# Optimization experiments

Measured on AMD Instinct MI355X. Metric: run time of the kernel, lower is better.

Reference implementation:

```python
import jax, jax.numpy as jnp
import numpy as np

B, L, D = 8, 2048, 1024
PAD = 512  # trailing padded positions (zeros) to exercise the two padding masks


def setup_inputs() -> dict:
    key = jax.random.key(0)
    ks = jax.random.split(key, 11)
    q = jax.random.normal(ks[0], (B, L, D), dtype=jnp.float32)
    k = jax.random.normal(ks[1], (B, L, D), dtype=jnp.float32)
    v = jax.random.normal(ks[2], (B, L, D), dtype=jnp.float32)
    # zero-pad trailing positions (module infers masks from zero rows)
    q = q.at[:, L - PAD:, :].set(0.0)
    k = k.at[:, L - PAD:, :].set(0.0)
    v = v.at[:, L - PAD:, :].set(0.0)
    s = 1.0 / np.sqrt(D)
    Wq = jax.random.normal(ks[3], (D, D), dtype=jnp.float32) * s
    bq = jax.random.normal(ks[4], (D,), dtype=jnp.float32) * 0.01
    Wk = jax.random.normal(ks[5], (D, D), dtype=jnp.float32) * s
    bk = jax.random.normal(ks[6], (D,), dtype=jnp.float32) * 0.01
    Wv = jax.random.normal(ks[7], (D, D), dtype=jnp.float32) * s
    bv = jax.random.normal(ks[8], (D,), dtype=jnp.float32) * 0.01
    Wo = jax.random.normal(ks[9], (D, D), dtype=jnp.float32) * s
    bo = jax.random.normal(ks[10], (D,), dtype=jnp.float32) * 0.01
    return {"q": q, "k": k, "v": v, "Wq": Wq, "bq": bq, "Wk": Wk, "bk": bk,
            "Wv": Wv, "bv": bv, "Wo": Wo, "bo": bo}


def reference(q, k, v, Wq, bq, Wk, bk, Wv, bv, Wo, bo):
    # masks computed from raw (pre-projection) q, k, exactly like padding_mask_k/_q
    # bmm(ones_like(q), k^T)[b,i,j] == sum_d k[b,j,d]  -> mask where k row sums to 0
    attn_mask = (jnp.sum(k, axis=-1) == 0.0)[:, None, :]      # [B,1,Lk] -> broadcast [B,Lq,Lk]
    softmax_mask = (jnp.sum(q, axis=-1) == 0.0)[:, :, None]    # [B,Lq,1]

    qp = q @ Wq.T + bq  # torch Linear: x W^T + b
    kp = k @ Wk.T + bk
    vp = v @ Wv.T + bv

    scale = vp.shape[-1] ** -0.5  # original overwrites passed `scale`
    att = jnp.einsum('bqd,bkd->bqk', qp, kp) * scale           # [B,Lq,Lk]
    att = jnp.where(attn_mask, -jnp.inf, att)
    att = jax.nn.softmax(att, axis=-1)
    att = jnp.where(softmax_mask, 0.0, att)

    out = jnp.einsum('bqk,bkd->bqd', att, vp)                  # [B,Lq,D]
    out = out @ Wo.T + bo
    x = out + qp  # residual uses the PROJECTED q
    # LayerNorm, elementwise_affine=False, eps=1e-5
    mu = jnp.mean(x, axis=-1, keepdims=True)
    var = jnp.mean(jnp.square(x - mu), axis=-1, keepdims=True)
    return (x - mu) / jnp.sqrt(var + 1e-5)
```

## Files before the change

### kernel.cpp

```cpp
#include <hip/hip_runtime.h>
#include <stdint.h>

typedef unsigned short u16;
typedef __attribute__((ext_vector_type(8))) short short8;
typedef __attribute__((ext_vector_type(4))) float f32x4;

#define B_ 8
#define L_ 2048
#define D_ 1024

__device__ __forceinline__ u16 f2bf(float f) {
    unsigned int u = __float_as_uint(f);
    u = u + 0x7FFFu + ((u >> 16) & 1u);
    return (u16)(u >> 16);
}
__device__ __forceinline__ float bf2f(u16 h) {
    return __uint_as_float(((unsigned int)h) << 16);
}

struct CM3 {
    const float* s[3];
    u16* d[3];
    int* m[3];
};
__global__ __launch_bounds__(256) void convmask3_kernel(CM3 c) {
    int sel = blockIdx.y;
    const float* x = c.s[sel];
    u16* xb = c.d[sel];
    int* mask = c.m[sel];
    long row = blockIdx.x;
    int t = threadIdx.x;
    float4 v = ((const float4*)(x + row * D_))[t];
    ushort4 o;
    o.x = f2bf(v.x); o.y = f2bf(v.y); o.z = f2bf(v.z); o.w = f2bf(v.w);
    ((ushort4*)(xb + row * D_))[t] = o;
    float s = v.x + v.y + v.z + v.w;
    #pragma unroll
    for (int off = 32; off; off >>= 1) s += __shfl_down(s, off);
    __shared__ float sh[4];
    if ((t & 63) == 0) sh[t >> 6] = s;
    __syncthreads();
    if (t == 0) {
        float tot = sh[0] + sh[1] + sh[2] + sh[3];
        mask[row] = (tot == 0.0f) ? 1 : 0;
    }
}

struct Ptr4 { const float* s0; const float* s1; const float* s2; const float* s3; };
__global__ __launch_bounds__(256) void convert4_kernel(Ptr4 p, u16* __restrict__ dst) {
    const float* srcs[4] = {p.s0, p.s1, p.s2, p.s3};
    const float* src = srcs[blockIdx.y];
    u16* d = dst + (size_t)blockIdx.y * D_ * D_;
    int i = blockIdx.x * 256 + threadIdx.x;
    float4 v = ((const float4*)src)[i];
    ushort4 o;
    o.x = f2bf(v.x); o.y = f2bf(v.y); o.z = f2bf(v.z); o.w = f2bf(v.w);
    ((ushort4*)d)[i] = o;
}

__global__ __launch_bounds__(256) void flags_kernel(const int* __restrict__ mq,
                                                    const int* __restrict__ mk,
                                                    const int* __restrict__ mv,
                                                    int* __restrict__ q256,
                                                    int* __restrict__ k256,
                                                    int* __restrict__ v256,
                                                    int* __restrict__ k128,
                                                    int* __restrict__ k32) {
    int b = blockIdx.x, t = threadIdx.x;
    const int* src; int* dst; int g; int n;
    if (b < 64)       { src = mq; dst = q256; g = b;       n = 256; }
    else if (b < 128) { src = mk; dst = k256; g = b - 64;  n = 256; }
    else if (b < 192) { src = mv; dst = v256; g = b - 128; n = 256; }
    else if (b < 320) { src = mk; dst = k128; g = b - 192; n = 128; }
    else              { src = mk; dst = k32;  g = b - 320; n = 32;  }
    int val = (t < n) ? src[(long)g * n + t] : 1;
    __shared__ int sh;
    if (t == 0) sh = 1;
    __syncthreads();
    if (!val) sh = 0;
    __syncthreads();
    if (t == 0) dst[g] = sh;
}

__global__ __launch_bounds__(512) void packbits_kernel(const int* __restrict__ k32,
                                                       unsigned long long* __restrict__ kb) {
    int t = threadIdx.x;
    int b = t >> 6;
    int bit = t & 63;
    unsigned long long m = __ballot(k32[b * 64 + bit] == 0);
    if (bit == 0) kb[b] = m;
}

__device__ __forceinline__ void async_cp16(const void* g, void* l) {
    __builtin_amdgcn_global_load_lds((const __attribute__((address_space(1))) unsigned int*)g,
                                     (__attribute__((address_space(3))) unsigned int*)l,
                                     16, 0, 0);
}

struct P3 {
    const u16* A[3];
    u16* C[3];
    const float* bias[3];
    const int* rs[3];
};

#define GBM 256
#define GBN 256
#define GBK 32

#define STAGE(step, slot)                                                   \
    do {                                                                    \
        const u16* pa_ = gA + (long)(step) * GBK;                           \
        const u16* pb_ = gB + (long)(step) * GBK;                           \
        u16* la_ = &LDS[(slot)][0] + t * 8;                                 \
        async_cp16(pa_, la_);                                               \
        async_cp16(pa_ + 128 * (long)K, la_ + 4096);                        \
        async_cp16(pb_, la_ + 8192);                                        \
        async_cp16(pb_ + 128 * (long)K, la_ + 12288);                       \
    } while (0)

template <int MODE>
__global__ __launch_bounds__(512, 2) void gemm_nt(const u16* __restrict__ A,
                                                  const u16* __restrict__ Bm,
                                                  void* __restrict__ C,
                                                  const float* __restrict__ bias,
                                                  const u16* __restrict__ resid,
                                                  const int* __restrict__ maskk,
                                                  int N, int K,
                                                  long strideA, long strideB, long strideC,
                                                  float scale,
                                                  const int* __restrict__ rowskip,
                                                  const int* __restrict__ colskip,
                                                  const unsigned long long* __restrict__ kbits,
                                                  int mblocks, int nblocks,
                                                  P3 p3) {
    __shared__ __align__(16) u16 LDS[4][16384];

    int t = threadIdx.x;
    int lane = t & 63;
    int wave = t >> 6;
    int wr = wave >> 2;
    int wc = wave & 3;
    long m0 = (long)blockIdx.x * GBM;
    long n0 = (long)blockIdx.y * GBN;

    const u16* Ab;
    const u16* Bb;
    char* Cb;
    const float* biasp = bias;
    const int* rs;
    int rsidx;
    if (MODE == 0) {
        int z = blockIdx.z;
        Ab = p3.A[z];
        Bb = Bm + (long)z * D_ * D_;
        Cb = (char*)p3.C[z];
        biasp = p3.bias[z];
        rs = p3.rs[z];
        rsidx = blockIdx.x;
    } else {
        Ab = A + (long)blockIdx.z * strideA;
        Bb = Bm + (long)blockIdx.z * strideB;
        Cb = (char*)C + (long)blockIdx.z * strideC;
        rs = rowskip;
        rsidx = blockIdx.z * mblocks + blockIdx.x;
    }
    const int* mk = (MODE == 1) ? (maskk + (long)blockIdx.z * N) : nullptr;

    bool skipK = false;
    if (rs && rs[rsidx]) skipK = true;
    if (MODE == 1 && colskip && colskip[blockIdx.z * nblocks + blockIdx.y]) skipK = true;

    f32x4 acc[8][4] = {};

    int srow = t >> 2;
    int kc = ((t & 3) ^ ((t >> 3) & 3)) * 8;
    const u16* gA = Ab + (m0 + srow) * (long)K + kc;
    const u16* gB = Bb + (n0 + srow) * (long)K + kc;

    int sw = ((lane >> 4) ^ ((lane >> 1) & 3)) * 8;
    int arow0 = wr * 128 + (lane & 15);
    int brow0 = wc * 64 + (lane & 15);

    if (!skipK) {
        unsigned long long bs = 0;
        int NT;
        if (MODE == 2) {
            bs = kbits[blockIdx.z];
            NT = __popcll(bs);
        } else {
            NT = K / GBK;
        }

        int npro = NT < 3 ? NT : 3;
        for (int i = 0; i < npro; i++) {
            int st = i;
            if (MODE == 2) { st = __builtin_ctzll(bs); bs &= bs - 1; }
            STAGE(st, i);
        }
        int nstaged = npro;

        for (int tt = 0; tt < NT; tt++) {
            int rem = NT - 1 - tt;
            if (rem > 1)      asm volatile("s_waitcnt vmcnt(8)" ::: "memory");
            else if (rem == 1) asm volatile("s_waitcnt vmcnt(4)" ::: "memory");
            else               asm volatile("s_waitcnt vmcnt(0)" ::: "memory");
            __builtin_amdgcn_s_barrier();
            asm volatile("" ::: "memory");

            if (nstaged < NT) {
                int st = nstaged;
                if (MODE == 2) { st = __builtin_ctzll(bs); bs &= bs - 1; }
                STAGE(st, nstaged & 3);
                nstaged++;
            }

            const u16* As_ = &LDS[tt & 3][0];
            const u16* Bs_ = As_ + 8192;
            short8 bfr[4], af[4];
            #pragma unroll
            for (int j = 0; j < 4; j++)
                bfr[j] = *(const short8*)&Bs_[(brow0 + j * 16) * GBK + sw];
            #pragma unroll
            for (int i = 0; i < 4; i++)
                af[i] = *(const short8*)&As_[(arow0 + i * 16) * GBK + sw];
            __builtin_amdgcn_s_setprio(1);
            #pragma unroll
            for (int i = 0; i < 4; i++)
                #pragma unroll
                for (int j = 0; j < 4; j++)
                    acc[i][j] = __builtin_amdgcn_mfma_f32_16x16x32_bf16(af[i], bfr[j],
                                                                        acc[i][j], 0, 0, 0);
            __builtin_amdgcn_s_setprio(0);
            #pragma unroll
            for (int i = 0; i < 4; i++)
                af[i] = *(const short8*)&As_[(arow0 + 64 + i * 16) * GBK + sw];
            __builtin_amdgcn_s_setprio(1);
            #pragma unroll
            for (int i = 0; i < 4; i++)
                #pragma unroll
                for (int j = 0; j < 4; j++)
                    acc[4 + i][j] = __builtin_amdgcn_mfma_f32_16x16x32_bf16(af[i], bfr[j],
                                                                            acc[4 + i][j], 0, 0, 0);
            __builtin_amdgcn_s_setprio(0);
        }
    }

    long crow0 = m0 + wr * 128;
    long ccol0 = n0 + wc * 64;
    #pragma unroll
    for (int i = 0; i < 8; i++) {
        #pragma unroll
        for (int j = 0; j < 4; j++) {
            long row = crow0 + i * 16 + (lane >> 4) * 4;
            long col = ccol0 + j * 16 + (lane & 15);
            #pragma unroll
            for (int r = 0; r < 4; r++) {
                float vv = acc[i][j][r];
                long rr = row + r;
                if (MODE == 0) {
                    ((u16*)Cb)[rr * N + col] = f2bf(vv + biasp[col]);
                } else if (MODE == 1) {
                    float s = mk[col] ? -1e30f : vv * scale;
                    ((u16*)Cb)[rr * N + col] = f2bf(s);
                } else if (MODE == 2) {
                    ((u16*)Cb)[rr * N + col] = f2bf(vv);
                } else {
                    float x = vv + biasp[col] + bf2f(resid[rr * (long)N + col]);
                    ((u16*)Cb)[rr * N + col] = f2bf(x);
                }
            }
        }
    }
}

__global__ __launch_bounds__(256) void softmax_kernel(const u16* __restrict__ S,
                                                      u16* __restrict__ P,
                                                      const int* __restrict__ maskq) {
    long row = blockIdx.x;
    int t = threadIdx.x;
    const u16* Sr = S + row * L_;
    u16* Pr = P + row * L_;

    if (maskq[row]) {
        short8 z = {};
        *(short8*)&Pr[t * 8] = z;
        return;
    }

    short8 raw = *(const short8*)&Sr[t * 8];
    float s[8];
    #pragma unroll
    for (int e = 0; e < 8; e++) s[e] = bf2f((u16)raw[e]);

    float mx = s[0];
    #pragma unroll
    for (int e = 1; e < 8; e++) mx = fmaxf(mx, s[e]);
    #pragma unroll
    for (int off = 32; off; off >>= 1) mx = fmaxf(mx, __shfl_down(mx, off));
    __shared__ float sh[4];
    if ((t & 63) == 0) sh[t >> 6] = mx;
    __syncthreads();
    mx = fmaxf(fmaxf(sh[0], sh[1]), fmaxf(sh[2], sh[3]));
    __syncthreads();

    float e8[8], sum = 0.f;
    #pragma unroll
    for (int e = 0; e < 8; e++) { e8[e] = __expf(s[e] - mx); sum += e8[e]; }
    #pragma unroll
    for (int off = 32; off; off >>= 1) sum += __shfl_down(sum, off);
    if ((t & 63) == 0) sh[t >> 6] = sum;
    __syncthreads();
    sum = sh[0] + sh[1] + sh[2] + sh[3];
    float inv = 1.0f / sum;

    short8 o;
    #pragma unroll
    for (int e = 0; e < 8; e++) o[e] = (short)f2bf(e8[e] * inv);
    *(short8*)&Pr[t * 8] = o;
}

__global__ __launch_bounds__(256) void transpose_k(const u16* __restrict__ src,
                                                   u16* __restrict__ dst) {
    __shared__ u16 tile[32][34];
    long b = blockIdx.z;
    const u16* s = src + b * (long)L_ * D_;
    u16* d = dst + b * (long)L_ * D_;
    int gx = blockIdx.x * 32;
    int gy = blockIdx.y * 32;
    int tx = threadIdx.x, ty = threadIdx.y;
    #pragma unroll
    for (int r = 0; r < 32; r += 8)
        tile[ty + r][tx] = s[(long)(gy + ty + r) * D_ + gx + tx];
    __syncthreads();
    #pragma unroll
    for (int r = 0; r < 32; r += 8)
        d[(long)(gx + ty + r) * L_ + gy + tx] = tile[tx][ty + r];
}

__global__ __launch_bounds__(256) void layernorm_kernel(const u16* __restrict__ X,
                                                        float* __restrict__ O) {
    long row = blockIdx.x;
    int t = threadIdx.x;
    ushort4 u = ((const ushort4*)(X + row * D_))[t];
    float x0 = bf2f(u.x), x1 = bf2f(u.y), x2 = bf2f(u.z), x3 = bf2f(u.w);
    float s = x0 + x1 + x2 + x3;
    #pragma unroll
    for (int off = 32; off; off >>= 1) s += __shfl_down(s, off);
    __shared__ float sh[4];
    if ((t & 63) == 0) sh[t >> 6] = s;
    __syncthreads();
    float mu = (sh[0] + sh[1] + sh[2] + sh[3]) * (1.0f / D_);
    __syncthreads();

    float d0 = x0 - mu, d1 = x1 - mu, d2 = x2 - mu, d3 = x3 - mu;
    float ss = d0 * d0 + d1 * d1 + d2 * d2 + d3 * d3;
    #pragma unroll
    for (int off = 32; off; off >>= 1) ss += __shfl_down(ss, off);
    if ((t & 63) == 0) sh[t >> 6] = ss;
    __syncthreads();
    float var = (sh[0] + sh[1] + sh[2] + sh[3]) * (1.0f / D_);
    float rs = rsqrtf(var + 1e-5f);

    float4 o;
    o.x = d0 * rs; o.y = d1 * rs; o.z = d2 * rs; o.w = d3 * rs;
    ((float4*)(O + row * D_))[t] = o;
}

extern "C" void kernel_launch(void* const* d_in, const int* in_sizes, int n_in,
                              void* d_out, int out_size, void* d_ws, size_t ws_size,
                              hipStream_t stream) {
    const float* q  = (const float*)d_in[0];
    const float* k  = (const float*)d_in[1];
    const float* v  = (const float*)d_in[2];
    const float* Wq = (const float*)d_in[3];
    const float* bq = (const float*)d_in[4];
    const float* Wk = (const float*)d_in[5];
    const float* bk = (const float*)d_in[6];
    const float* Wv = (const float*)d_in[7];
    const float* bv = (const float*)d_in[8];
    const float* Wo = (const float*)d_in[9];
    const float* bo = (const float*)d_in[10];
    float* out = (float*)d_out;

    char* ws = (char*)d_ws;
    const size_t SZ = (size_t)B_ * L_ * D_ * 2;

    u16* qb   = (u16*)(ws + 0 * SZ);
    u16* kb   = (u16*)(ws + 1 * SZ);
    u16* vb   = (u16*)(ws + 2 * SZ);
    u16* vpb  = (u16*)(ws + 3 * SZ);
    u16* Sbuf = (u16*)(ws + 0 * SZ);
    u16* Pbuf = (u16*)(ws + 2 * SZ);
    u16* Obuf = (u16*)(ws + 0 * SZ);
    u16* Xbuf = (u16*)(ws + 2 * SZ);
    char* p = ws + 4 * SZ;
    u16* qpb = (u16*)p; p += SZ;
    u16* kpb = (u16*)p; p += SZ;
    u16* vpT = (u16*)p; p += SZ;
    u16* Wqb = (u16*)p; p += (size_t)D_ * D_ * 2;
    u16* Wkb = (u16*)p; p += (size_t)D_ * D_ * 2;
    u16* Wvb = (u16*)p; p += (size_t)D_ * D_ * 2;
    u16* Wob = (u16*)p; p += (size_t)D_ * D_ * 2;
    int* maskq = (int*)p; p += (size_t)B_ * L_ * 4;
    int* maskk = (int*)p; p += (size_t)B_ * L_ * 4;
    int* maskv = (int*)p; p += (size_t)B_ * L_ * 4;
    int* q256 = (int*)p; p += 64 * 4;
    int* k256 = (int*)p; p += 64 * 4;
    int* v256 = (int*)p; p += 64 * 4;
    int* kmask128 = (int*)p; p += 128 * 4;
    int* kmask32  = (int*)p; p += 512 * 4;
    unsigned long long* kbits = (unsigned long long*)p; p += 8 * 8;

    P3 noP3 = {};

    CM3 cm;
    cm.s[0] = q;  cm.s[1] = k;  cm.s[2] = v;
    cm.d[0] = qb; cm.d[1] = kb; cm.d[2] = vb;
    cm.m[0] = maskq; cm.m[1] = maskk; cm.m[2] = maskv;
    convmask3_kernel<<<dim3(B_ * L_, 3), 256, 0, stream>>>(cm);
    Ptr4 wp{Wq, Wk, Wv, Wo};
    convert4_kernel<<<dim3(D_ * D_ / 4 / 256, 4), 256, 0, stream>>>(wp, Wqb);
    flags_kernel<<<832, 256, 0, stream>>>(maskq, maskk, maskv, q256, k256, v256, kmask128, kmask32);
    packbits_kernel<<<1, 512, 0, stream>>>(kmask32, kbits);

    P3 pj;
    pj.A[0] = qb;  pj.A[1] = kb;  pj.A[2] = vb;
    pj.C[0] = qpb; pj.C[1] = kpb; pj.C[2] = vpb;
    pj.bias[0] = bq; pj.bias[1] = bk; pj.bias[2] = bv;
    pj.rs[0] = q256; pj.rs[1] = k256; pj.rs[2] = v256;
    gemm_nt<0><<<dim3(B_ * L_ / GBM, D_ / GBN, 3), 512, 0, stream>>>(
        nullptr, Wqb, nullptr, nullptr, nullptr, nullptr, D_, D_, 0, 0, 0, 0.f,
        nullptr, nullptr, nullptr, 0, 4, pj);

    transpose_k<<<dim3(D_ / 32, L_ / 32, B_), dim3(32, 8), 0, stream>>>(vpb, vpT);

    gemm_nt<1><<<dim3(L_ / GBM, L_ / GBN, B_), 512, 0, stream>>>(
        qpb, kpb, Sbuf, nullptr, nullptr, maskk, L_, D_,
        (long)L_ * D_, (long)L_ * D_, (long)L_ * L_ * 2, 0.03125f,
        q256, k256, nullptr, L_ / GBM, L_ / GBN, noP3);

    softmax_kernel<<<B_ * L_, 256, 0, stream>>>(Sbuf, Pbuf, maskq);

    gemm_nt<2><<<dim3(L_ / GBM, D_ / GBN, B_), 512, 0, stream>>>(
        Pbuf, vpT, Obuf, nullptr, nullptr, nullptr, D_, L_,
        (long)L_ * L_, (long)D_ * L_, (long)L_ * D_ * 2, 0.f,
        q256, nullptr, kbits, L_ / GBM, D_ / GBN, noP3);

    gemm_nt<3><<<dim3(B_ * L_ / GBM, D_ / GBN, 1), 512, 0, stream>>>(
        Obuf, Wob, Xbuf, bo, qpb, nullptr, D_, D_, 0, 0, 0, 0.f,
        q256, nullptr, nullptr, B_ * L_ / GBM, D_ / GBN, noP3);

    layernorm_kernel<<<B_ * L_, 256, 0, stream>>>(Xbuf, out);
}
```

Before: 550.7 us.

## Restructure GEMM to BK=64 double-buffered quadrant pipeline with interleaved loads

The GEMM main loop changes from a 4-slot BK=32 ring to a 2-buffer BK=64 scheme. Each wave now computes four 64x32 quadrants, with LDS reads, async global-to-LDS copies and MFMA phases interleaved between barriers, and a new 8-way XOR swizzle. In step with the larger K tile, the skip bitmask is repacked to 32 bits per batch, each bit covering two 32-wide chunks. The aim is more overlap of memory traffic with MFMA work and fewer loop iterations. The cost is more barriers per iteration and fragile waitcnt accounting.

```diff
diff --git a/kernel.cpp b/kernel.cpp
--- a/kernel.cpp
+++ b/kernel.cpp
@@ -82,13 +82,14 @@
     if (t == 0) dst[g] = sh;
 }
 
-__global__ __launch_bounds__(512) void packbits_kernel(const int* __restrict__ k32,
+__global__ __launch_bounds__(256) void packbits_kernel(const int* __restrict__ k32,
                                                        unsigned long long* __restrict__ kb) {
     int t = threadIdx.x;
-    int b = t >> 6;
-    int bit = t & 63;
-    unsigned long long m = __ballot(k32[b * 64 + bit] == 0);
-    if (bit == 0) kb[b] = m;
+    int b = t >> 5;
+    int i = t & 31;
+    bool act = (k32[b * 64 + 2 * i] == 0) || (k32[b * 64 + 2 * i + 1] == 0);
+    unsigned long long m = __ballot(act);
+    if (i == 0) kb[b] = (b & 1) ? (m >> 32) : (m & 0xffffffffULL);
 }
 
 __device__ __forceinline__ void async_cp16(const void* g, void* l) {
@@ -106,17 +107,54 @@
 
 #define GBM 256
 #define GBN 256
-#define GBK 32
-
-#define STAGE(step, slot)                                                   \
-    do {                                                                    \
-        const u16* pa_ = gA + (long)(step) * GBK;                           \
-        const u16* pb_ = gB + (long)(step) * GBK;                           \
-        u16* la_ = &LDS[(slot)][0] + t * 8;                                 \
-        async_cp16(pa_, la_);                                               \
-        async_cp16(pa_ + 128 * (long)K, la_ + 4096);                        \
-        async_cp16(pb_, la_ + 8192);                                        \
-        async_cp16(pb_ + 128 * (long)K, la_ + 12288);                       \
+#define GBK 64
+
+#define STG(BUF, HALF, STEP)                                                     \
+    do {                                                                         \
+        const u16* g_ = (((HALF) < 2) ? gA0 : gB0) +                             \
+                        (long)((HALF) & 1) * 128 * (long)K + (long)(STEP) * GBK; \
+        u16* l_ = &LDS[BUF][HALF][t * 8];                                        \
+        async_cp16(g_, l_);                                                      \
+        async_cp16(g_ + 64 * (long)K, l_ + 4096);                                \
+    } while (0)
+
+#define DSA(QM)                                                                  \
+    _Pragma("unroll")                                                            \
+    for (int i_ = 0; i_ < 4; i_++) {                                             \
+        af[i_][0] = *(const short8*)&LDS[buf][QM][aoff + i_ * 1024 + c0];        \
+        af[i_][1] = *(const short8*)&LDS[buf][QM][aoff + i_ * 1024 + c1];        \
+    }
+#define DSB(QN)                                                                  \
+    _Pragma("unroll")                                                            \
+    for (int j_ = 0; j_ < 2; j_++) {                                             \
+        bf[j_][0] = *(const short8*)&LDS[buf][2 + (QN)][boff + j_ * 1024 + c0];  \
+        bf[j_][1] = *(const short8*)&LDS[buf][2 + (QN)][boff + j_ * 1024 + c1];  \
+    }
+#define MF(QM, QN)                                                               \
+    __builtin_amdgcn_s_setprio(1);                                               \
+    _Pragma("unroll")                                                            \
+    for (int i_ = 0; i_ < 4; i_++) {                                             \
+        _Pragma("unroll")                                                        \
+        for (int j_ = 0; j_ < 2; j_++) {                                         \
+            acc[QM][QN][i_][j_] = __builtin_amdgcn_mfma_f32_16x16x32_bf16(       \
+                af[i_][0], bf[j_][0], acc[QM][QN][i_][j_], 0, 0, 0);             \
+            acc[QM][QN][i_][j_] = __builtin_amdgcn_mfma_f32_16x16x32_bf16(       \
+                af[i_][1], bf[j_][1], acc[QM][QN][i_][j_], 0, 0, 0);             \
+        }                                                                        \
+    }                                                                            \
+    __builtin_amdgcn_s_setprio(0);
+
+#define BAR_IN                                                  \
+    do {                                                        \
+        asm volatile("" ::: "memory");                          \
+        __builtin_amdgcn_s_barrier();                           \
+        asm volatile("s_waitcnt lgkmcnt(0)" ::: "memory");      \
+        __builtin_amdgcn_sched_barrier(0);                      \
+    } while (0)
+#define BAR_OUT                                                 \
+    do {                                                        \
+        asm volatile("" ::: "memory");                          \
+        __builtin_amdgcn_s_barrier();                           \
     } while (0)
 
 template <int MODE>
@@ -134,13 +172,13 @@
                                                   const unsigned long long* __restrict__ kbits,
                                                   int mblocks, int nblocks,
                                                   P3 p3) {
-    __shared__ __align__(16) u16 LDS[4][16384];
+    __shared__ __align__(16) u16 LDS[2][4][8192];
 
     int t = threadIdx.x;
     int lane = t & 63;
     int wave = t >> 6;
-    int wr = wave >> 2;
-    int wc = wave & 3;
+    int wr2 = wave >> 2;
+    int wc4 = wave & 3;
     long m0 = (long)blockIdx.x * GBM;
     long n0 = (long)blockIdx.y * GBN;
 
@@ -171,16 +209,16 @@
     if (rs && rs[rsidx]) skipK = true;
     if (MODE == 1 && colskip && colskip[blockIdx.z * nblocks + blockIdx.y]) skipK = true;
 
-    f32x4 acc[8][4] = {};
-
-    int srow = t >> 2;
-    int kc = ((t & 3) ^ ((t >> 3) & 3)) * 8;
-    const u16* gA = Ab + (m0 + srow) * (long)K + kc;
-    const u16* gB = Bb + (n0 + srow) * (long)K + kc;
-
-    int sw = ((lane >> 4) ^ ((lane >> 1) & 3)) * 8;
-    int arow0 = wr * 128 + (lane & 15);
-    int brow0 = wc * 64 + (lane & 15);
+    f32x4 acc[2][2][4][2] = {};
+
+    int kcx = ((t & 7) ^ ((t >> 3) & 7)) * 8;
+    const u16* gA0 = Ab + (m0 + (t >> 3)) * (long)K + kcx;
+    const u16* gB0 = Bb + (n0 + (t >> 3)) * (long)K + kcx;
+
+    int aoff = (wr2 * 64 + (lane & 15)) * 64;
+    int boff = (wc4 * 32 + (lane & 15)) * 64;
+    int c0 = ((lane >> 4) ^ (lane & 7)) * 8;
+    int c1 = ((4 + (lane >> 4)) ^ (lane & 7)) * 8;
 
     if (!skipK) {
         unsigned long long bs = 0;
@@ -192,82 +230,93 @@
             NT = K / GBK;
         }
 
-        int npro = NT < 3 ? NT : 3;
-        for (int i = 0; i < npro; i++) {
-            int st = i;
-            if (MODE == 2) { st = __builtin_ctzll(bs); bs &= bs - 1; }
-            STAGE(st, i);
+        if (NT > 0) {
+            int st0, st1 = 0, st2 = 0;
+            if (MODE == 2) { st0 = __builtin_ctzll(bs); bs &= bs - 1; } else st0 = 0;
+
+            STG(0, 0, st0);
+            STG(0, 3, st0);
+            STG(0, 1, st0);
+            STG(0, 2, st0);
+            if (NT >= 2) {
+                if (MODE == 2) { st1 = __builtin_ctzll(bs); bs &= bs - 1; } else st1 = 1;
+                STG(1, 0, st1);
+                STG(1, 3, st1);
+                asm volatile("s_waitcnt vmcnt(4)" ::: "memory");
+            } else {
+                asm volatile("s_waitcnt vmcnt(0)" ::: "memory");
+            }
+            asm volatile("" ::: "memory");
+            __builtin_amdgcn_s_barrier();
+
+            if (NT >= 3) {
+                if (MODE == 2) { st2 = __builtin_ctzll(bs); bs &= bs - 1; } else st2 = 2;
+            }
+
+            for (int tt = 0; tt < NT; tt++) {
+                int buf = tt & 1;
+                int bufN = buf ^ 1;
+                bool s0 = (tt + 1 < NT);
+                bool s2 = (tt + 2 < NT);
+                short8 af[4][2], bf[2][2];
+
+                DSA(0); DSB(0);
+                if (s0) { STG(bufN, 1, st1); STG(bufN, 2, st1); }
+                asm volatile("s_waitcnt lgkmcnt(8)" ::: "memory");
+                BAR_IN; MF(0, 0); BAR_OUT;
+
+                DSB(1);
+                BAR_IN; MF(0, 1); BAR_OUT;
+
+                DSA(1);
+                if (s2) STG(buf, 0, st2);
+                BAR_IN; MF(1, 1); BAR_OUT;
+
+                DSB(0);
+                if (s2) {
+                    STG(buf, 3, st2);
+                    asm volatile("s_waitcnt vmcnt(4)" ::: "memory");
+                } else if (s0) {
+                    asm volatile("s_waitcnt vmcnt(0)" ::: "memory");
+                }
+                BAR_IN; MF(1, 0); BAR_OUT;
+
+                st1 = st2;
+                if (MODE == 2) {
+                    if (tt + 3 < NT) { st2 = __builtin_ctzll(bs); bs &= bs - 1; }
+                } else {
+                    st2 = tt + 3;
+                }
+            }
         }
-        int nstaged = npro;
-
-        for (int tt = 0; tt < NT; tt++) {
-            int rem = NT - 1 - tt;
-            if (rem > 1)      asm volatile("s_waitcnt vmcnt(8)" ::: "memory");
-            else if (rem == 1) asm volatile("s_waitcnt vmcnt(4)" ::: "memory");
-            else               asm volatile("s_waitcnt vmcnt(0)" ::: "memory");
-            __builtin_amdgcn_s_barrier();
-            asm volatile("" ::: "memory");
-
-            if (nstaged < NT) {
-                int st = nstaged;
-                if (MODE == 2) { st = __builtin_ctzll(bs); bs &= bs - 1; }
-                STAGE(st, nstaged & 3);
-                nstaged++;
-            }
-
-            const u16* As_ = &LDS[tt & 3][0];
-            const u16* Bs_ = As_ + 8192;
-            short8 bfr[4], af[4];
+    }
+
+    #pragma unroll
+    for (int QM = 0; QM < 2; QM++) {
+        #pragma unroll
+        for (int QN = 0; QN < 2; QN++) {
             #pragma unroll
-            for (int j = 0; j < 4; j++)
-                bfr[j] = *(const short8*)&Bs_[(brow0 + j * 16) * GBK + sw];
-            #pragma unroll
-            for (int i = 0; i < 4; i++)
-                af[i] = *(const short8*)&As_[(arow0 + i * 16) * GBK + sw];
-            __builtin_amdgcn_s_setprio(1);
-            #pragma unroll
-            for (int i = 0; i < 4; i++)
+            for (int i = 0; i < 4; i++) {
                 #pragma unroll
-                for (int j = 0; j < 4; j++)
-                    acc[i][j] = __builtin_amdgcn_mfma_f32_16x16x32_bf16(af[i], bfr[j],
-                                                                        acc[i][j], 0, 0, 0);
-            __builtin_amdgcn_s_setprio(0);
-            #pragma unroll
-            for (int i = 0; i < 4; i++)
-                af[i] = *(const short8*)&As_[(arow0 + 64 + i * 16) * GBK + sw];
-            __builtin_amdgcn_s_setprio(1);
-            #pragma unroll
-            for (int i = 0; i < 4; i++)
-                #pragma unroll
-                for (int j = 0; j < 4; j++)
-                    acc[4 + i][j] = __builtin_amdgcn_mfma_f32_16x16x32_bf16(af[i], bfr[j],
-                                                                            acc[4 + i][j], 0, 0, 0);
-            __builtin_amdgcn_s_setprio(0);
-        }
-    }
-
-    long crow0 = m0 + wr * 128;
-    long ccol0 = n0 + wc * 64;
-    #pragma unroll
-    for (int i = 0; i < 8; i++) {
-        #pragma unroll
-        for (int j = 0; j < 4; j++) {
-            long row = crow0 + i * 16 + (lane >> 4) * 4;
-            long col = ccol0 + j * 16 + (lane & 15);
-            #pragma unroll
-            for (int r = 0; r < 4; r++) {
-                float vv = acc[i][j][r];
-                long rr = row + r;
-                if (MODE == 0) {
-                    ((u16*)Cb)[rr * N + col] = f2bf(vv + biasp[col]);
-                } else if (MODE == 1) {
-                    float s = mk[col] ? -1e30f : vv * scale;
-                    ((u16*)Cb)[rr * N + col] = f2bf(s);
-                } else if (MODE == 2) {
-                    ((u16*)Cb)[rr * N + col] = f2bf(vv);
-                } else {
-                    float x = vv + biasp[col] + bf2f(resid[rr * (long)N + col]);
-                    ((u16*)Cb)[rr * N + col] = f2bf(x);
+                for (int j = 0; j < 2; j++) {
+                    long row = m0 + QM * 128 + wr2 * 64 + i * 16 + (lane >> 4) * 4;
+                    long col = n0 + QN * 128 + wc4 * 32 + j * 16 + (lane & 15);
+                    #pragma unroll
+                    for (int r = 0; r < 4; r++) {
+                        float vv = acc[QM][QN][i][j][r];
+                        long rr = row + r;
+                        if (MODE == 0) {
+                            ((u16*)Cb)[rr * N + col] = f2bf(vv + biasp[col]);
+                        } else if (MODE == 1) {
+                            float s = mk[col] ? -1e30f : vv * scale;
+                            ((u16*)Cb)[rr * N + col] = f2bf(s);
+                        } else if (MODE == 2) {
+                            ((u16*)Cb)[rr * N + col] = f2bf(vv);
+                        } else {
+                            float x = vv + biasp[col] + bf2f(resid[rr * (long)N + col]);
+                            ((u16*)Cb)[rr * N + col] = f2bf(x);
+                        }
+                    }
                 }
             }
         }
@@ -422,7 +471,7 @@
     Ptr4 wp{Wq, Wk, Wv, Wo};
     convert4_kernel<<<dim3(D_ * D_ / 4 / 256, 4), 256, 0, stream>>>(wp, Wqb);
     flags_kernel<<<832, 256, 0, stream>>>(maskq, maskk, maskv, q256, k256, v256, kmask128, kmask32);
-    packbits_kernel<<<1, 512, 0, stream>>>(kmask32, kbits);
+    packbits_kernel<<<1, 256, 0, stream>>>(kmask32, kbits);
 
     P3 pj;
     pj.A[0] = qb;  pj.A[1] = kb;  pj.A[2] = vb;
```

Result: no change. 550.4 us (-0.1%).
